# Kernel tuning notes

Hardware: AMD Instinct MI355X
Metric: run time of the kernel (lower is better)

## Reference

```python
import jax, jax.numpy as jnp
import numpy as np

# DSVT single-stage config (mmdet3d DSVT-Pillar, Waymo)
SPARSE_SHAPE = (468, 468, 1)            # (x, y, z)
WIN_SHAPES = [(12, 12, 1), (24, 24, 1)]  # base window, hybrid window (hybrid_factor=[2,2,1])
SHIFTS = [(0, 0, 0), (6, 6, 0)]          # shift_list per shift id
SET_SIZE = 36
NUM_BLOCKS = 4
DIM = 192
BN_EPS = 1e-5


def get_window_coors(coors, sparse_shape, window_shape, shift):
    ssx, ssy, ssz = sparse_shape
    wx, wy, wz = window_shape
    mx = int(np.ceil(ssx / wx) + 1)
    my = int(np.ceil(ssy / wy) + 1)
    mz = int(np.ceil(ssz / wz) + 1)
    sx, sy, sz = shift
    if ssz == wz:
        sz = 0
    scx = coors[:, 3] + sx
    scy = coors[:, 2] + sy
    scz = coors[:, 1] + sz
    batch_win_inds = (coors[:, 0] * (mx * my * mz)
                      + (scx // wx) * my * mz + (scy // wy) * mz + (scz // wz))
    coors_in_win = jnp.stack([scz % wz, scy % wy, scx % wx], axis=-1)  # (z, y, x)
    return batch_win_inds, coors_in_win


def get_inner_win_inds(win_inds):
    # rank of each voxel inside its window (stable order), like get_inner_win_inds
    n = win_inds.shape[0]
    order = jnp.argsort(win_inds)  # jnp.argsort is stable
    sw = win_inds[order]
    ar = jnp.arange(n, dtype=win_inds.dtype)
    is_start = jnp.concatenate([jnp.ones((1,), bool), sw[1:] != sw[:-1]])
    start = jax.lax.cummax(jnp.where(is_start, ar, 0), axis=0)
    return jnp.zeros(n, win_inds.dtype).at[order].set(ar - start)


def get_set_single_shift(batch_win_inds, coors_in_win, window_shape, set_size):
    wx, wy, wz = window_shape
    max_voxel = wx * wy * wz
    n = batch_win_inds.shape[0]
    uniq, contig = jnp.unique(batch_win_inds, return_inverse=True)
    contig = contig.reshape(-1).astype(jnp.int32)
    win_num = int(uniq.shape[0])
    vnum_per_win = jnp.bincount(contig, length=win_num).astype(jnp.int32)
    setnum_per_win = (vnum_per_win + set_size - 1) // set_size  # ceil
    # get_continous_inds
    set_win_inds = jnp.repeat(jnp.arange(win_num, dtype=jnp.int32), setnum_per_win)
    excl = jnp.concatenate([jnp.zeros((1,), jnp.int32),
                            jnp.cumsum(setnum_per_win)[:-1].astype(jnp.int32)])
    set_inds_in_win = jnp.arange(set_win_inds.shape[0], dtype=jnp.int32) - excl[set_win_inds]

    # Eq.3 of DSVT: evenly spread the voxels of each window over its sets
    base_idx = jnp.arange(set_size, dtype=jnp.int32)
    num = (set_inds_in_win[:, None] * set_size + base_idx) * vnum_per_win[set_win_inds][:, None]
    den = (setnum_per_win[set_win_inds] * set_size)[:, None]
    select_idx = num // den + set_win_inds[:, None] * max_voxel  # [set_num, set_size]

    inner = get_inner_win_inds(contig)
    order1 = jnp.argsort(contig * max_voxel + inner)

    z = coors_in_win[:, 0].astype(jnp.int32)
    y = coors_in_win[:, 1].astype(jnp.int32)
    x = coors_in_win[:, 2].astype(jnp.int32)

    def partition(key):
        order2 = jnp.argsort(key)
        inner_s = jnp.full((n,), -1, jnp.int32).at[order2].set(inner[order1])
        in_batch = inner_s + max_voxel * contig
        padding = jnp.full((win_num * max_voxel,), -1, jnp.int32).at[in_batch].set(
            jnp.arange(n, dtype=jnp.int32))
        return padding[select_idx]

    key_sorty = contig * max_voxel + y * (wx * wz) + x * wz + z
    key_sortx = contig * max_voxel + x * (wy * wz) + y * wz + z
    return jnp.stack([partition(key_sorty), partition(key_sortx)], axis=0)


def set_mask(set_voxel_inds):
    prefix = jnp.roll(set_voxel_inds, 1, axis=-1).at[:, :, 0].set(-1)
    return set_voxel_inds == prefix


def compute_locations(voxel_coords):
    infos, locs = [], []
    win_x, win_y = WIN_SHAPES[0][0], WIN_SHAPES[0][1]  # pos-embed uses base window, 2D (win_z==1)
    for s in range(2):
        bwi, ciw = get_window_coors(voxel_coords, SPARSE_SHAPE, WIN_SHAPES[s], SHIFTS[s])
        infos.append((bwi, ciw))
        xx = ciw[:, 2].astype(jnp.float32) - win_x / 2
        yy = ciw[:, 1].astype(jnp.float32) - win_y / 2
        locs.append(jnp.stack([xx, yy], axis=-1))
    return infos, jnp.stack(locs)  # [2, N, 2]


def _pos_embed(w1, b1, g, bt, w2, b2, loc):
    # Linear -> BatchNorm1d (train-mode batch stats) -> ReLU -> Linear
    h = loc @ w1 + b1
    mu = h.mean(0)
    var = h.var(0)
    h = (h - mu) * jax.lax.rsqrt(var + BN_EPS) * g + bt
    return jnp.maximum(h, 0.0) @ w2 + b2


def setup_inputs() -> dict:
    key = jax.random.key(0)
    B, NPB, GX, GY = 2, 30000, 468, 468
    rng = np.random.default_rng(0)
    coords = []
    for b in range(B):
        lin = rng.choice(GX * GY, size=NPB, replace=False)  # unique occupied pillars
        coords.append(np.stack([np.full(NPB, b), np.zeros(NPB), lin // GX, lin % GX], axis=1))
    voxel_coords = jnp.asarray(np.concatenate(coords, 0), dtype=jnp.int32)  # (bid, z, y, x)
    N = B * NPB
    K = 2 * NUM_BLOCKS
    ks = jax.random.split(key, 3)
    return {
        'voxel_features': jax.random.normal(ks[0], (N, DIM), jnp.float32),
        'voxel_coords': voxel_coords,
        'pe_w1': jax.random.normal(ks[1], (K, 2, DIM), jnp.float32) * 0.02,
        'pe_b1': jnp.zeros((K, DIM), jnp.float32),
        'pe_gamma': jnp.ones((K, DIM), jnp.float32),
        'pe_beta': jnp.zeros((K, DIM), jnp.float32),
        'pe_w2': jax.random.normal(ks[2], (K, DIM, DIM), jnp.float32) * 0.02,
        'pe_b2': jnp.zeros((K, DIM), jnp.float32),
    }


def reference(voxel_features, voxel_coords, pe_w1, pe_b1, pe_gamma, pe_beta, pe_w2, pe_b2):
    infos, locs = compute_locations(voxel_coords)
    set_inds0 = get_set_single_shift(infos[0][0], infos[0][1], WIN_SHAPES[0], SET_SIZE)
    set_inds1 = get_set_single_shift(infos[1][0], infos[1][1], WIN_SHAPES[1], SET_SIZE)
    mask0 = set_mask(set_inds0)
    mask1 = set_mask(set_inds1)
    # 4 blocks x 2 shifts learned position embeddings; location depends only on shift
    loc_k = locs[jnp.arange(2 * NUM_BLOCKS) % 2]  # [8, N, 2]
    pos_embeds = jax.vmap(_pos_embed)(pe_w1, pe_b1, pe_gamma, pe_beta, pe_w2, pe_b2, loc_k)
    return (voxel_features, voxel_coords, set_inds0, mask0, set_inds1, mask1, pos_embeds)
```

## Files before the change

kernel.cpp:

```cpp
#include <hip/hip_runtime.h>
#include <stdint.h>

#define DIM 192
#define SET_SIZE 36

#define W0 6400
#define MV0 144
#define W1 1764
#define MV1 576

#define CAP_S0 6144
#define CAP_S1 4096

#define OFF_CNT0     0
#define OFF_CNT1     6400
#define OFF_MOM      8164
#define OFF_S0       8174
#define OFF_S1       8175
#define OFF_ZERO_END 8176
#define OFF_SETBASE0 8192
#define OFF_SETBASE1 14592
#define OFF_SETWIN0  16356
#define OFF_SETWIN1  22500
#define OFF_CELL0    26596
#define OFF_CELL1    86596
#define OFF_SLOTY0   146596
#define OFF_SLOTX0   1068196
#define OFF_SLOTY1   1989796
#define OFF_SLOTX1   3005860
#define OFF_TABLE    4021924
#define WS_TOTAL     4906660

__global__ void voxel_pass(const int* __restrict__ coords, int N, int* __restrict__ ws) {
    int v = blockIdx.x * blockDim.x + threadIdx.x;
    __shared__ int sm[10];
    if (threadIdx.x < 10) sm[threadIdx.x] = 0;
    __syncthreads();
    if (v < N) {
        int b = coords[v * 4 + 0];
        int z = coords[v * 4 + 1];
        int y = coords[v * 4 + 2];
        int x = coords[v * 4 + 3];
        int xin0 = x % 12, yin0 = y % 12;
        int w0 = b * 3200 + (x / 12) * 80 + (y / 12) * 2 + z;
        atomicAdd(&ws[OFF_CNT0 + w0], 1);
        ws[OFF_SLOTY0 + w0 * MV0 + yin0 * 12 + xin0] = v;
        ws[OFF_SLOTX0 + w0 * MV0 + xin0 * 12 + yin0] = v;
        ws[OFF_CELL0 + v] = yin0 * 12 + xin0;
        int sx = x + 6, sy = y + 6;
        int xin1 = sx % 24, yin1 = sy % 24;
        int w1 = b * 882 + (sx / 24) * 42 + (sy / 24) * 2 + z;
        atomicAdd(&ws[OFF_CNT1 + w1], 1);
        ws[OFF_SLOTY1 + w1 * MV1 + yin1 * 24 + xin1] = v;
        ws[OFF_SLOTX1 + w1 * MV1 + xin1 * 24 + yin1] = v;
        ws[OFF_CELL1 + v] = yin1 * 24 + xin1;
        int xx0 = xin0 - 6, yy0 = yin0 - 6;
        int xx1 = xin1 - 6, yy1 = yin1 - 6;
        atomicAdd(&sm[0], xx0); atomicAdd(&sm[1], yy0);
        atomicAdd(&sm[2], xx0 * xx0); atomicAdd(&sm[3], yy0 * yy0); atomicAdd(&sm[4], xx0 * yy0);
        atomicAdd(&sm[5], xx1); atomicAdd(&sm[6], yy1);
        atomicAdd(&sm[7], xx1 * xx1); atomicAdd(&sm[8], yy1 * yy1); atomicAdd(&sm[9], xx1 * yy1);
    }
    __syncthreads();
    if (threadIdx.x < 10) atomicAdd(&ws[OFF_MOM + threadIdx.x], sm[threadIdx.x]);
}

__global__ void scan_sets(const int* __restrict__ cnt, int W,
                          int* __restrict__ setBase, int* __restrict__ setWin,
                          int* __restrict__ S_out, int cap) {
    __shared__ int sm[256];
    int tid = threadIdx.x;
    int chunk = (W + 255) >> 8;
    int lo = tid * chunk;
    int hi = lo + chunk; if (hi > W) hi = W; if (lo > W) lo = W;
    int local = 0;
    for (int w = lo; w < hi; w++) local += (cnt[w] + SET_SIZE - 1) / SET_SIZE;
    sm[tid] = local;
    __syncthreads();
    for (int off = 1; off < 256; off <<= 1) {
        int t = (tid >= off) ? sm[tid - off] : 0;
        __syncthreads();
        sm[tid] += t;
        __syncthreads();
    }
    int base = sm[tid] - local;
    if (tid == 255) {
        int S = sm[255];
        if (S > cap) S = cap;
        *S_out = S;
    }
    for (int w = lo; w < hi; w++) {
        setBase[w] = base;
        int sn = (cnt[w] + SET_SIZE - 1) / SET_SIZE;
        for (int s = 0; s < sn; s++) {
            int idx = base + s;
            if (idx < cap) setWin[idx] = w;
        }
        base += sn;
    }
}

__global__ void compact_windows(int* __restrict__ slotY, int* __restrict__ slotX, int MV) {
    int w = blockIdx.x;
    int lane = threadIdx.x;
    for (int pass = 0; pass < 2; pass++) {
        int* slot = pass ? slotX : slotY;
        int base = 0;
        for (int p0 = 0; p0 < MV; p0 += 64) {
            int p = p0 + lane;
            int v = (p < MV) ? slot[(size_t)w * MV + p] : -1;
            bool occ = v >= 0;
            unsigned long long m = __ballot(occ);
            int rank = __popcll(m & ((1ull << lane) - 1ull));
            if (occ) slot[(size_t)w * MV + base + rank] = v;
            base += __popcll(m);
        }
    }
}

__global__ void write_sets(const int* __restrict__ S_ptr, const int* __restrict__ setWin,
                           const int* __restrict__ setBase, const int* __restrict__ cnt,
                           const int* __restrict__ sortedY, const int* __restrict__ sortedX,
                           int MV, int cap, float* __restrict__ outArea,
                           const int* __restrict__ S_prev ) {
    long long tid = (long long)blockIdx.x * blockDim.x + threadIdx.x;
    int S = *S_ptr;
    int j = (int)(tid % SET_SIZE);
    long long t = tid / SET_SIZE;
    int q = (int)(t % cap);
    int branch = (int)(t / cap);
    if (branch >= 2 || q >= S) return;
    long long sOff = 0;
    if (S_prev) sOff = 4LL * SET_SIZE * (long long)(*S_prev);
    int w = setWin[q];
    int i = q - setBase[w];
    int vnum = cnt[w];
    int setnum = (vnum + SET_SIZE - 1) / SET_SIZE;
    int den = setnum * SET_SIZE;
    int r  = ((i * SET_SIZE + j) * vnum) / den;
    int rp = (j > 0) ? (((i * SET_SIZE + j - 1) * vnum) / den) : -1;
    const int* sorted = branch ? sortedX : sortedY;
    int vox = sorted[(size_t)w * MV + r];
    long long idx = (long long)branch * S * SET_SIZE + (long long)q * SET_SIZE + j;
    outArea[sOff + idx] = (float)vox;
    outArea[sOff + 2LL * S * SET_SIZE + idx] = (r == rp) ? 1.0f : 0.0f;
}

__global__ void build_table(const float* __restrict__ w1, const float* __restrict__ gamma,
                            const float* __restrict__ beta, const float* __restrict__ w2,
                            const float* __restrict__ b2, const int* __restrict__ mom,
                            float* __restrict__ table, int N) {
    int k = blockIdx.x / MV1;
    int cell = blockIdx.x % MV1;
    int shift = k & 1;
    int wdim = shift ? 24 : 12;
    if (cell >= wdim * wdim) return;
    int j = threadIdx.x;
    const int* m = mom + shift * 5;
    double invN = 1.0 / (double)N;
    double mx = m[0] * invN, my = m[1] * invN;
    double vx = m[2] * invN - mx * mx;
    double vy = m[3] * invN - my * my;
    double cxy = m[4] * invN - mx * my;
    int cy = cell / wdim, cx = cell % wdim;
    double xx = (double)(cx - 6), yy = (double)(cy - 6);
    float w10 = w1[(k * 2 + 0) * DIM + j];
    float w11 = w1[(k * 2 + 1) * DIM + j];
    double var = (double)w10 * w10 * vx + (double)w11 * w11 * vy + 2.0 * (double)w10 * w11 * cxy;
    double rs = 1.0 / sqrt(var + 1e-5);
    double hn = ((xx - mx) * (double)w10 + (yy - my) * (double)w11) * rs * (double)gamma[k * DIM + j]
                + (double)beta[k * DIM + j];
    float hr = hn > 0.0 ? (float)hn : 0.0f;
    __shared__ float sh[DIM];
    sh[j] = hr;
    __syncthreads();
    float acc = b2[k * DIM + j];
    const float* w2k = w2 + (size_t)k * DIM * DIM;
    #pragma unroll 8
    for (int i = 0; i < DIM; i++) acc += sh[i] * w2k[i * DIM + j];
    table[((size_t)k * MV1 + cell) * DIM + j] = acc;
}

__global__ void scatter_pe(const float4* __restrict__ table, const int* __restrict__ cell0,
                           const int* __restrict__ cell1, float4* __restrict__ out, int N) {
    long long tid = (long long)blockIdx.x * blockDim.x + threadIdx.x;
    long long total = 8LL * N * (DIM / 4);
    if (tid >= total) return;
    int q = (int)(tid % (DIM / 4));
    long long t = tid / (DIM / 4);
    int v = (int)(t % N);
    int k = (int)(t / N);
    int cell = (k & 1) ? cell1[v] : cell0[v];
    out[tid] = table[((size_t)k * MV1 + cell) * (DIM / 4) + q];
}

__global__ void coords_to_float(const int* __restrict__ c, float* __restrict__ o, int n) {
    int i = blockIdx.x * blockDim.x + threadIdx.x;
    if (i < n) o[i] = (float)c[i];
}

extern "C" void kernel_launch(void* const* d_in, const int* in_sizes, int n_in,
                              void* d_out, int out_size, void* d_ws, size_t ws_size,
                              hipStream_t stream) {
    const float* feat  = (const float*)d_in[0];
    const int* coords  = (const int*)d_in[1];
    const float* w1    = (const float*)d_in[2];
    const float* gamma = (const float*)d_in[4];
    const float* beta  = (const float*)d_in[5];
    const float* w2    = (const float*)d_in[6];
    const float* b2    = (const float*)d_in[7];
    int N = in_sizes[1] / 4;
    int* ws = (int*)d_ws;
    float* out = (float*)d_out;

    hipMemsetAsync(ws, 0, (size_t)OFF_ZERO_END * sizeof(int), stream);
    hipMemsetAsync(ws + OFF_SLOTY0, 0xFF, (size_t)(OFF_TABLE - OFF_SLOTY0) * sizeof(int), stream);

    voxel_pass<<<(N + 255) / 256, 256, 0, stream>>>(coords, N, ws);

    scan_sets<<<1, 256, 0, stream>>>(ws + OFF_CNT0, W0, ws + OFF_SETBASE0, ws + OFF_SETWIN0,
                                     ws + OFF_S0, CAP_S0);
    scan_sets<<<1, 256, 0, stream>>>(ws + OFF_CNT1, W1, ws + OFF_SETBASE1, ws + OFF_SETWIN1,
                                     ws + OFF_S1, CAP_S1);

    compact_windows<<<W0, 64, 0, stream>>>(ws + OFF_SLOTY0, ws + OFF_SLOTX0, MV0);
    compact_windows<<<W1, 64, 0, stream>>>(ws + OFF_SLOTY1, ws + OFF_SLOTX1, MV1);

    long long off2 = (long long)N * DIM + (long long)N * 4;
    {
        long long threads = 2LL * CAP_S0 * SET_SIZE;
        write_sets<<<(int)((threads + 255) / 256), 256, 0, stream>>>(
            ws + OFF_S0, ws + OFF_SETWIN0, ws + OFF_SETBASE0, ws + OFF_CNT0,
            ws + OFF_SLOTY0, ws + OFF_SLOTX0, MV0, CAP_S0, out + off2, nullptr);
    }
    {
        long long threads = 2LL * CAP_S1 * SET_SIZE;
        write_sets<<<(int)((threads + 255) / 256), 256, 0, stream>>>(
            ws + OFF_S1, ws + OFF_SETWIN1, ws + OFF_SETBASE1, ws + OFF_CNT1,
            ws + OFF_SLOTY1, ws + OFF_SLOTX1, MV1, CAP_S1, out + off2, ws + OFF_S0);
    }

    build_table<<<8 * MV1, DIM, 0, stream>>>(w1, gamma, beta, w2, b2,
                                             ws + OFF_MOM, (float*)(ws + OFF_TABLE), N);

    long long off6 = (long long)out_size - 8LL * N * DIM;
    {
        long long t4 = 8LL * N * (DIM / 4);
        scatter_pe<<<(int)((t4 + 255) / 256), 256, 0, stream>>>(
            (const float4*)(ws + OFF_TABLE), ws + OFF_CELL0, ws + OFF_CELL1,
            (float4*)(out + off6), N);
    }

    coords_to_float<<<(N * 4 + 255) / 256, 256, 0, stream>>>(coords, out + (long long)N * DIM, N * 4);
    hipMemcpyAsync(out, feat, (size_t)N * DIM * sizeof(float), hipMemcpyDeviceToDevice, stream);
}
```

Before: 539.7 us.

## Fuse pipeline stages: merged scans, compact+write sets, tiled table build, single output kernel

Replaces the shared-memory atomics in voxel_pass with wavefront shuffle reductions and loads coords as int4. Both set scans now run in one launch, and the setWin array is dropped. Window compaction and set writing are fused into a per-window kernel that compacts into LDS, removing two global round trips. The PE table build processes 8 cells per block to reuse each w2 load, and the scatter, feature copy and coords conversion are merged into one 2D-grid kernel. Fewer launches and less memory traffic are the aim, at the cost of more complex per-block work and possible imbalance across windows.

```diff
diff --git a/kernel.cpp b/kernel.cpp
--- a/kernel.cpp
+++ b/kernel.cpp
@@ -31,16 +31,12 @@
 #define OFF_TABLE    4021924
 #define WS_TOTAL     4906660
 
-__global__ void voxel_pass(const int* __restrict__ coords, int N, int* __restrict__ ws) {
+__global__ void voxel_pass(const int4* __restrict__ coords, int N, int* __restrict__ ws) {
     int v = blockIdx.x * blockDim.x + threadIdx.x;
-    __shared__ int sm[10];
-    if (threadIdx.x < 10) sm[threadIdx.x] = 0;
-    __syncthreads();
+    int xx0 = 0, yy0 = 0, xx1 = 0, yy1 = 0;
     if (v < N) {
-        int b = coords[v * 4 + 0];
-        int z = coords[v * 4 + 1];
-        int y = coords[v * 4 + 2];
-        int x = coords[v * 4 + 3];
+        int4 c = coords[v];
+        int b = c.x, z = c.y, y = c.z, x = c.w;
         int xin0 = x % 12, yin0 = y % 12;
         int w0 = b * 3200 + (x / 12) * 80 + (y / 12) * 2 + z;
         atomicAdd(&ws[OFF_CNT0 + w0], 1);
@@ -54,21 +50,28 @@
         ws[OFF_SLOTY1 + w1 * MV1 + yin1 * 24 + xin1] = v;
         ws[OFF_SLOTX1 + w1 * MV1 + xin1 * 24 + yin1] = v;
         ws[OFF_CELL1 + v] = yin1 * 24 + xin1;
-        int xx0 = xin0 - 6, yy0 = yin0 - 6;
-        int xx1 = xin1 - 6, yy1 = yin1 - 6;
-        atomicAdd(&sm[0], xx0); atomicAdd(&sm[1], yy0);
-        atomicAdd(&sm[2], xx0 * xx0); atomicAdd(&sm[3], yy0 * yy0); atomicAdd(&sm[4], xx0 * yy0);
-        atomicAdd(&sm[5], xx1); atomicAdd(&sm[6], yy1);
-        atomicAdd(&sm[7], xx1 * xx1); atomicAdd(&sm[8], yy1 * yy1); atomicAdd(&sm[9], xx1 * yy1);
-    }
-    __syncthreads();
-    if (threadIdx.x < 10) atomicAdd(&ws[OFF_MOM + threadIdx.x], sm[threadIdx.x]);
-}
-
-__global__ void scan_sets(const int* __restrict__ cnt, int W,
-                          int* __restrict__ setBase, int* __restrict__ setWin,
-                          int* __restrict__ S_out, int cap) {
+        xx0 = xin0 - 6; yy0 = yin0 - 6;
+        xx1 = xin1 - 6; yy1 = yin1 - 6;
+    }
+    int mvals[10] = {xx0, yy0, xx0 * xx0, yy0 * yy0, xx0 * yy0,
+                     xx1, yy1, xx1 * xx1, yy1 * yy1, xx1 * yy1};
+    #pragma unroll
+    for (int m = 0; m < 10; m++) {
+        int s = mvals[m];
+        #pragma unroll
+        for (int off = 32; off > 0; off >>= 1) s += __shfl_down(s, off);
+        if ((threadIdx.x & 63) == 0) atomicAdd(&ws[OFF_MOM + m], s);
+    }
+}
+
+__global__ void scan_both(int* __restrict__ ws) {
     __shared__ int sm[256];
+    int shift = blockIdx.x;
+    const int W = shift ? W1 : W0;
+    const int cap = shift ? CAP_S1 : CAP_S0;
+    const int* cnt = ws + (shift ? OFF_CNT1 : OFF_CNT0);
+    int* setBase = ws + (shift ? OFF_SETBASE1 : OFF_SETBASE0);
+    int* S_out   = ws + (shift ? OFF_S1 : OFF_S0);
     int tid = threadIdx.x;
     int chunk = (W + 255) >> 8;
     int lo = tid * chunk;
@@ -89,72 +92,68 @@
         if (S > cap) S = cap;
         *S_out = S;
     }
-    for (int w = lo; w < hi; w++) {
-        setBase[w] = base;
-        int sn = (cnt[w] + SET_SIZE - 1) / SET_SIZE;
-        for (int s = 0; s < sn; s++) {
-            int idx = base + s;
-            if (idx < cap) setWin[idx] = w;
-        }
-        base += sn;
-    }
-}
-
-__global__ void compact_windows(int* __restrict__ slotY, int* __restrict__ slotX, int MV) {
-    int w = blockIdx.x;
-    int lane = threadIdx.x;
-    for (int pass = 0; pass < 2; pass++) {
-        int* slot = pass ? slotX : slotY;
+    for (int w = lo; w < hi; w++) setBase[w] = (base += 0, base), base += (cnt[w] + SET_SIZE - 1) / SET_SIZE;
+}
+
+__global__ void __launch_bounds__(128)
+compact_write(const int* __restrict__ ws, float* __restrict__ outArea) {
+    __shared__ int sY[MV1], sX[MV1];
+    int bw = blockIdx.x;
+    int shift = (bw >= W0) ? 1 : 0;
+    int w = shift ? (bw - W0) : bw;
+    int cnt = ws[(shift ? OFF_CNT1 : OFF_CNT0) + w];
+    if (cnt == 0) return;
+    int MV = shift ? MV1 : MV0;
+    const int* slotY = ws + (shift ? OFF_SLOTY1 : OFF_SLOTY0) + (size_t)w * MV;
+    const int* slotX = ws + (shift ? OFF_SLOTX1 : OFF_SLOTX0) + (size_t)w * MV;
+    int lane = threadIdx.x & 63;
+    int wsel = threadIdx.x >> 6;
+    {
+        const int* slot = wsel ? slotX : slotY;
+        int* dst = wsel ? sX : sY;
         int base = 0;
         for (int p0 = 0; p0 < MV; p0 += 64) {
             int p = p0 + lane;
-            int v = (p < MV) ? slot[(size_t)w * MV + p] : -1;
+            int v = (p < MV) ? slot[p] : -1;
             bool occ = v >= 0;
             unsigned long long m = __ballot(occ);
             int rank = __popcll(m & ((1ull << lane) - 1ull));
-            if (occ) slot[(size_t)w * MV + base + rank] = v;
+            if (occ) dst[base + rank] = v;
             base += __popcll(m);
         }
     }
-}
-
-__global__ void write_sets(const int* __restrict__ S_ptr, const int* __restrict__ setWin,
-                           const int* __restrict__ setBase, const int* __restrict__ cnt,
-                           const int* __restrict__ sortedY, const int* __restrict__ sortedX,
-                           int MV, int cap, float* __restrict__ outArea,
-                           const int* __restrict__ S_prev ) {
-    long long tid = (long long)blockIdx.x * blockDim.x + threadIdx.x;
-    int S = *S_ptr;
-    int j = (int)(tid % SET_SIZE);
-    long long t = tid / SET_SIZE;
-    int q = (int)(t % cap);
-    int branch = (int)(t / cap);
-    if (branch >= 2 || q >= S) return;
-    long long sOff = 0;
-    if (S_prev) sOff = 4LL * SET_SIZE * (long long)(*S_prev);
-    int w = setWin[q];
-    int i = q - setBase[w];
-    int vnum = cnt[w];
-    int setnum = (vnum + SET_SIZE - 1) / SET_SIZE;
+    __syncthreads();
+    int S = ws[shift ? OFF_S1 : OFF_S0];
+    long long sOff = shift ? 4LL * SET_SIZE * (long long)ws[OFF_S0] : 0;
+    int sb = ws[(shift ? OFF_SETBASE1 : OFF_SETBASE0) + w];
+    int setnum = (cnt + SET_SIZE - 1) / SET_SIZE;
     int den = setnum * SET_SIZE;
-    int r  = ((i * SET_SIZE + j) * vnum) / den;
-    int rp = (j > 0) ? (((i * SET_SIZE + j - 1) * vnum) / den) : -1;
-    const int* sorted = branch ? sortedX : sortedY;
-    int vox = sorted[(size_t)w * MV + r];
-    long long idx = (long long)branch * S * SET_SIZE + (long long)q * SET_SIZE + j;
-    outArea[sOff + idx] = (float)vox;
-    outArea[sOff + 2LL * S * SET_SIZE + idx] = (r == rp) ? 1.0f : 0.0f;
-}
-
-__global__ void build_table(const float* __restrict__ w1, const float* __restrict__ gamma,
-                            const float* __restrict__ beta, const float* __restrict__ w2,
-                            const float* __restrict__ b2, const int* __restrict__ mom,
-                            float* __restrict__ table, int N) {
-    int k = blockIdx.x / MV1;
-    int cell = blockIdx.x % MV1;
+    int total = 2 * den;
+    for (int e = threadIdx.x; e < total; e += 128) {
+        int branch = (e >= den) ? 1 : 0;
+        int rem = e - branch * den;
+        int i = rem / 36, j = rem - i * 36;
+        int q = sb + i;
+        if (q >= S) continue;
+        int r  = (rem * cnt) / den;
+        int rp = (j > 0) ? (((rem - 1) * cnt) / den) : -1;
+        int vox = branch ? sX[r] : sY[r];
+        long long idx = (long long)branch * S * SET_SIZE + (long long)q * SET_SIZE + j;
+        outArea[sOff + idx] = (float)vox;
+        outArea[sOff + 2LL * S * SET_SIZE + idx] = (r == rp) ? 1.0f : 0.0f;
+    }
+}
+
+__global__ void __launch_bounds__(192)
+build_table(const float* __restrict__ w1, const float* __restrict__ gamma,
+            const float* __restrict__ beta, const float* __restrict__ w2,
+            const float* __restrict__ b2, const int* __restrict__ mom,
+            float* __restrict__ table, int N) {
+    int bid = blockIdx.x;
+    int k, tile, wdim;
+    if (bid < 72) { k = (bid / 18) * 2;            tile = bid % 18; wdim = 12; }
+    else { int b = bid - 72; k = (b / 72) * 2 + 1; tile = b % 72;   wdim = 24; }
     int shift = k & 1;
-    int wdim = shift ? 24 : 12;
-    if (cell >= wdim * wdim) return;
     int j = threadIdx.x;
     const int* m = mom + shift * 5;
     double invN = 1.0 / (double)N;
@@ -162,41 +161,57 @@
     double vx = m[2] * invN - mx * mx;
     double vy = m[3] * invN - my * my;
     double cxy = m[4] * invN - mx * my;
-    int cy = cell / wdim, cx = cell % wdim;
-    double xx = (double)(cx - 6), yy = (double)(cy - 6);
     float w10 = w1[(k * 2 + 0) * DIM + j];
     float w11 = w1[(k * 2 + 1) * DIM + j];
     double var = (double)w10 * w10 * vx + (double)w11 * w11 * vy + 2.0 * (double)w10 * w11 * cxy;
     double rs = 1.0 / sqrt(var + 1e-5);
-    double hn = ((xx - mx) * (double)w10 + (yy - my) * (double)w11) * rs * (double)gamma[k * DIM + j]
-                + (double)beta[k * DIM + j];
-    float hr = hn > 0.0 ? (float)hn : 0.0f;
-    __shared__ float sh[DIM];
-    sh[j] = hr;
+    double gs = rs * (double)gamma[k * DIM + j];
+    double bt = (double)beta[k * DIM + j];
+    __shared__ float sh[8][DIM];
+    #pragma unroll
+    for (int c = 0; c < 8; c++) {
+        int cell = tile * 8 + c;
+        int cy = cell / wdim, cx = cell - cy * wdim;
+        double hn = (((double)(cx - 6) - mx) * (double)w10 +
+                     ((double)(cy - 6) - my) * (double)w11) * gs + bt;
+        sh[c][j] = hn > 0.0 ? (float)hn : 0.0f;
+    }
     __syncthreads();
-    float acc = b2[k * DIM + j];
+    float acc[8];
+    float bb = b2[k * DIM + j];
+    #pragma unroll
+    for (int c = 0; c < 8; c++) acc[c] = bb;
     const float* w2k = w2 + (size_t)k * DIM * DIM;
-    #pragma unroll 8
-    for (int i = 0; i < DIM; i++) acc += sh[i] * w2k[i * DIM + j];
-    table[((size_t)k * MV1 + cell) * DIM + j] = acc;
-}
-
-__global__ void scatter_pe(const float4* __restrict__ table, const int* __restrict__ cell0,
-                           const int* __restrict__ cell1, float4* __restrict__ out, int N) {
-    long long tid = (long long)blockIdx.x * blockDim.x + threadIdx.x;
-    long long total = 8LL * N * (DIM / 4);
-    if (tid >= total) return;
-    int q = (int)(tid % (DIM / 4));
-    long long t = tid / (DIM / 4);
-    int v = (int)(t % N);
-    int k = (int)(t / N);
-    int cell = (k & 1) ? cell1[v] : cell0[v];
-    out[tid] = table[((size_t)k * MV1 + cell) * (DIM / 4) + q];
-}
-
-__global__ void coords_to_float(const int* __restrict__ c, float* __restrict__ o, int n) {
-    int i = blockIdx.x * blockDim.x + threadIdx.x;
-    if (i < n) o[i] = (float)c[i];
+    for (int i = 0; i < DIM; i++) {
+        float wv = w2k[i * DIM + j];
+        #pragma unroll
+        for (int c = 0; c < 8; c++) acc[c] = fmaf(sh[c][i], wv, acc[c]);
+    }
+    #pragma unroll
+    for (int c = 0; c < 8; c++)
+        table[((size_t)k * MV1 + tile * 8 + c) * DIM + j] = acc[c];
+}
+
+__global__ void write_out(const float4* __restrict__ table, const int* __restrict__ cell0,
+                          const int* __restrict__ cell1, const float4* __restrict__ feat,
+                          const int4* __restrict__ coords, float4* __restrict__ outPe,
+                          float4* __restrict__ outFeat, float4* __restrict__ outCoords,
+                          int N) {
+    int t = blockIdx.x * 256 + threadIdx.x;
+    if (t >= N * 48) return;
+    int k = blockIdx.y;
+    if (k < 8) {
+        int v = t / 48;
+        int q = t - v * 48;
+        int cell = (k & 1) ? cell1[v] : cell0[v];
+        outPe[(size_t)k * N * 48 + t] = table[((size_t)k * MV1 + cell) * 48 + q];
+    } else {
+        outFeat[t] = feat[t];
+        if (t < N) {
+            int4 c = coords[t];
+            outCoords[t] = make_float4((float)c.x, (float)c.y, (float)c.z, (float)c.w);
+        }
+    }
 }
 
 extern "C" void kernel_launch(void* const* d_in, const int* in_sizes, int n_in,
@@ -216,41 +231,21 @@
     hipMemsetAsync(ws, 0, (size_t)OFF_ZERO_END * sizeof(int), stream);
     hipMemsetAsync(ws + OFF_SLOTY0, 0xFF, (size_t)(OFF_TABLE - OFF_SLOTY0) * sizeof(int), stream);
 
-    voxel_pass<<<(N + 255) / 256, 256, 0, stream>>>(coords, N, ws);
-
-    scan_sets<<<1, 256, 0, stream>>>(ws + OFF_CNT0, W0, ws + OFF_SETBASE0, ws + OFF_SETWIN0,
-                                     ws + OFF_S0, CAP_S0);
-    scan_sets<<<1, 256, 0, stream>>>(ws + OFF_CNT1, W1, ws + OFF_SETBASE1, ws + OFF_SETWIN1,
-                                     ws + OFF_S1, CAP_S1);
-
-    compact_windows<<<W0, 64, 0, stream>>>(ws + OFF_SLOTY0, ws + OFF_SLOTX0, MV0);
-    compact_windows<<<W1, 64, 0, stream>>>(ws + OFF_SLOTY1, ws + OFF_SLOTX1, MV1);
+    voxel_pass<<<(N + 255) / 256, 256, 0, stream>>>((const int4*)coords, N, ws);
+
+    scan_both<<<2, 256, 0, stream>>>(ws);
 
     long long off2 = (long long)N * DIM + (long long)N * 4;
-    {
-        long long threads = 2LL * CAP_S0 * SET_SIZE;
-        write_sets<<<(int)((threads + 255) / 256), 256, 0, stream>>>(
-            ws + OFF_S0, ws + OFF_SETWIN0, ws + OFF_SETBASE0, ws + OFF_CNT0,
-            ws + OFF_SLOTY0, ws + OFF_SLOTX0, MV0, CAP_S0, out + off2, nullptr);
-    }
-    {
-        long long threads = 2LL * CAP_S1 * SET_SIZE;
-        write_sets<<<(int)((threads + 255) / 256), 256, 0, stream>>>(
-            ws + OFF_S1, ws + OFF_SETWIN1, ws + OFF_SETBASE1, ws + OFF_CNT1,
-            ws + OFF_SLOTY1, ws + OFF_SLOTX1, MV1, CAP_S1, out + off2, ws + OFF_S0);
-    }
-
-    build_table<<<8 * MV1, DIM, 0, stream>>>(w1, gamma, beta, w2, b2,
-                                             ws + OFF_MOM, (float*)(ws + OFF_TABLE), N);
+    compact_write<<<W0 + W1, 128, 0, stream>>>(ws, out + off2);
+
+    build_table<<<4 * 18 + 4 * 72, DIM, 0, stream>>>(w1, gamma, beta, w2, b2,
+                                                     ws + OFF_MOM, (float*)(ws + OFF_TABLE), N);
 
     long long off6 = (long long)out_size - 8LL * N * DIM;
-    {
-        long long t4 = 8LL * N * (DIM / 4);
-        scatter_pe<<<(int)((t4 + 255) / 256), 256, 0, stream>>>(
-            (const float4*)(ws + OFF_TABLE), ws + OFF_CELL0, ws + OFF_CELL1,
-            (float4*)(out + off6), N);
-    }
-
-    coords_to_float<<<(N * 4 + 255) / 256, 256, 0, stream>>>(coords, out + (long long)N * DIM, N * 4);
-    hipMemcpyAsync(out, feat, (size_t)N * DIM * sizeof(float), hipMemcpyDeviceToDevice, stream);
-}
+    dim3 g((unsigned)((N * 48 + 255) / 256), 9);
+    write_out<<<g, 256, 0, stream>>>((const float4*)(ws + OFF_TABLE),
+                                     ws + OFF_CELL0, ws + OFF_CELL1,
+                                     (const float4*)feat, (const int4*)coords,
+                                     (float4*)(out + off6), (float4*)out,
+                                     (float4*)(out + (long long)N * DIM), N);
+}
```

Measured after the change: 598.3 us. 1.11x slower.
